# Performance work log

Measured on AMD Instinct MI355X. Metric: run time of the kernel, lower is better.

## Reference

```python
import jax, jax.numpy as jnp
import numpy as np


def setup_inputs() -> dict:
    key = jax.random.key(0)
    ks = jax.random.split(key, 7)
    B, S, D = 256, 1024, 128  # batch of sets, set size, n_input
    H = 256
    x = jax.random.normal(ks[0], (B, S, D), dtype=jnp.float32)
    # torch nn.Linear weights: [out_features, in_features], in = 2*layer_in
    W0 = jax.random.normal(ks[1], (H, 2 * D), dtype=jnp.float32) * 0.05
    b0 = jnp.zeros((H,), dtype=jnp.float32)
    W1 = jax.random.normal(ks[2], (H, 2 * H), dtype=jnp.float32) * 0.05
    b1 = jnp.zeros((H,), dtype=jnp.float32)
    W2 = jax.random.normal(ks[3], (H, 2 * H), dtype=jnp.float32) * 0.05
    b2 = jnp.zeros((H,), dtype=jnp.float32)
    return {"x": x, "W0": W0, "b0": b0, "W1": W1, "b1": b1, "W2": W2, "b2": b2}


def reference(x, W0, b0, W1, b1, W2, b2):
    # x: [B, S, D] batch of sets. Original loops over batch; we vmap.
    def apply_set(y):
        # y: [S, d]
        for W, b in ((W0, b0), (W1, b1), (W2, b2)):
            mean = jnp.mean(y, axis=0, keepdims=True)            # [1, d]
            mean = jnp.broadcast_to(mean, y.shape)               # [S, d]
            z = jnp.concatenate([y, mean], axis=1)               # [S, 2d]
            y = jnp.tanh(z @ W.T + b)                            # [S, out]
        return jnp.mean(y, axis=0)                               # [out]
    return jax.vmap(apply_set)(x)                                # [B, out]
```

## Files before the change

### kernel.cpp

```cpp
#include <hip/hip_runtime.h>
#include <hip/hip_bf16.h>

#define B_ 256
#define S_ 1024
#define D_ 128
#define H_ 256

typedef short short8 __attribute__((ext_vector_type(8)));
typedef float f32x4 __attribute__((ext_vector_type(4)));

__device__ unsigned short g_Wb0[H_ * D_];
__device__ unsigned short g_Wb1[H_ * H_];
__device__ unsigned short g_Wb2[H_ * H_];
__device__ float g_mean0[B_ * D_];
__device__ float g_colsum1[B_ * H_];
__device__ float g_colsum2[B_ * H_];

__device__ __forceinline__ unsigned short f2bf(float x) {
    union { float f; unsigned u; } v; v.f = x;
    unsigned r = v.u + 0x7FFFu + ((v.u >> 16) & 1u);
    return (unsigned short)(r >> 16);
}
__device__ __forceinline__ float bf2f(unsigned short h) {
    union { float f; unsigned u; } v; v.u = ((unsigned)h) << 16;
    return v.f;
}
__device__ __forceinline__ float fast_tanh(float x) {
    float e = __builtin_amdgcn_exp2f(x * 2.885390081777927f);
    float r = __builtin_amdgcn_rcpf(1.0f + e);
    return 1.0f - 2.0f * r;
}

__global__ __launch_bounds__(256) void prep_kernel(
    const float* __restrict__ W0, const float* __restrict__ W1,
    const float* __restrict__ W2)
{
    int i = blockIdx.x * 256 + threadIdx.x;
    if (i < H_ * D_) { g_Wb0[i] = f2bf(W0[(i >> 7) * 256 + (i & 127)]); return; }
    i -= H_ * D_;
    if (i < H_ * H_) { g_Wb1[i] = f2bf(W1[(i >> 8) * 512 + (i & 255)]); return; }
    i -= H_ * H_;
    if (i < H_ * H_) { g_Wb2[i] = f2bf(W2[(i >> 8) * 512 + (i & 255)]); return; }
}

__global__ __launch_bounds__(1024) void means0_kernel(const float* __restrict__ x)
{
    const int set = blockIdx.x, t = threadIdx.x;
    const int cg = t & 31, rg = t >> 5;
    const float* xb = x + (size_t)set * S_ * D_;
    f32x4 s = (f32x4){0.f, 0.f, 0.f, 0.f};
    #pragma unroll 8
    for (int i = 0; i < 32; ++i)
        s += *(const f32x4*)(xb + (rg + i * 32) * D_ + cg * 4);
    __shared__ f32x4 red[32][32];
    red[rg][cg] = s;
    __syncthreads();
    if (t < 32) {
        f32x4 a = red[0][t];
        #pragma unroll
        for (int g = 1; g < 32; ++g) a += red[g][t];
        #pragma unroll
        for (int c = 0; c < 4; ++c) g_mean0[set * D_ + t * 4 + c] = a[c];
    }
}

template <int LAYER>
__global__ __launch_bounds__(512, 2) void layer_kernel(
    const float* __restrict__ x, const float* __restrict__ W,
    const float* __restrict__ bias, unsigned short* __restrict__ y,
    float* __restrict__ out)
{
    constexpr int K  = (LAYER == 0) ? D_ : H_;
    constexpr int KS = K / 32;
    constexpr int SLOTS = K / 8;
    const int set = blockIdx.x;
    const int t = threadIdx.x;
    const int lane = t & 63, wave = t >> 6;
    const int l15 = lane & 15, quad = lane >> 4;

    __shared__ unsigned short W_lds[256 * K];
    __shared__ float mean_lds[K];
    __shared__ float c_lds[H_];
    __shared__ float colsum_lds[H_];
    __shared__ float cpart[512];

    const unsigned short* Wb = (LAYER == 0) ? g_Wb0 : (LAYER == 1) ? g_Wb1 : g_Wb2;
    const float* msrc = (LAYER == 0) ? g_mean0 : (LAYER == 1) ? g_colsum1 : g_colsum2;

    if (t < K)   mean_lds[t] = msrc[set * K + t] * (1.f / S_);
    if (t < H_)  colsum_lds[t] = 0.f;
    __syncthreads();

    {
        const int n = t >> 1, h = t & 1;
        #pragma unroll
        for (int i = 0; i < SLOTS / 2; ++i) {
            const int slot = h * (SLOTS / 2) + i;
            *(uint4*)(&W_lds[n * K + ((slot ^ (n & 7)) * 8)]) =
                *(const uint4*)(&Wb[n * K + slot * 8]);
        }
    }
    {
        const int j = t >> 1, h = t & 1;
        const float* wl = W + j * 2 * K + h * (K / 2);
        const float* wr = wl + K;
        float acc = 0.f;
        #pragma unroll 4
        for (int k = 0; k < K / 2; k += 4) {
            f32x4 a = *(const f32x4*)(wl + k);
            f32x4 b = *(const f32x4*)(wr + k);
            f32x4 m = *(const f32x4*)(&mean_lds[h * (K / 2) + k]);
            #pragma unroll
            for (int c = 0; c < 4; ++c)
                acc += m[c] * (b[c] + (a[c] - bf2f(f2bf(a[c]))));
        }
        cpart[t] = acc;
    }
    __syncthreads();
    if (t < H_) c_lds[t] = bias[t] + cpart[2 * t] + cpart[2 * t + 1];
    __syncthreads();

    for (int half = 0; half < 2; ++half) {
        const int rowbase = half * 512 + wave * 64;

        short8 a[4][KS];
        if (LAYER == 0) {
            const float* xb = x + ((size_t)set * S_ + rowbase) * D_;
            #pragma unroll
            for (int mf = 0; mf < 4; ++mf)
                #pragma unroll
                for (int ks = 0; ks < KS; ++ks) {
                    const float* p = xb + (mf * 16 + l15) * D_ + ks * 32 + quad * 8;
                    f32x4 v0 = *(const f32x4*)(p);
                    f32x4 v1 = *(const f32x4*)(p + 4);
                    short8 sv;
                    #pragma unroll
                    for (int c = 0; c < 4; ++c) {
                        sv[c]     = (short)f2bf(v0[c]);
                        sv[4 + c] = (short)f2bf(v1[c]);
                    }
                    a[mf][ks] = sv;
                }
        } else {
            const unsigned short* yb = y + ((size_t)set * S_ + rowbase) * H_;
            #pragma unroll
            for (int mf = 0; mf < 4; ++mf)
                #pragma unroll
                for (int ks = 0; ks < KS; ++ks)
                    a[mf][ks] = *(const short8*)(yb + (mf * 16 + l15) * H_ + ks * 32 + quad * 8);
        }

        for (int nt = 0; nt < 8; ++nt) {
            f32x4 acc[4][2];
            #pragma unroll
            for (int i = 0; i < 4; ++i) {
                acc[i][0] = (f32x4){0.f, 0.f, 0.f, 0.f};
                acc[i][1] = (f32x4){0.f, 0.f, 0.f, 0.f};
            }
            const int r0 = (nt * 32 + l15) * K;
            const int r1 = (nt * 32 + 16 + l15) * K;
            #pragma unroll
            for (int ks = 0; ks < KS; ++ks) {
                const int so = (((ks * 4 + quad) ^ (l15 & 7)) * 8);
                short8 b0 = *(const short8*)(&W_lds[r0 + so]);
                short8 b1 = *(const short8*)(&W_lds[r1 + so]);
                #pragma unroll
                for (int mf = 0; mf < 4; ++mf)
                    acc[mf][0] = __builtin_amdgcn_mfma_f32_16x16x32_bf16(a[mf][ks], b0, acc[mf][0], 0, 0, 0);
                #pragma unroll
                for (int mf = 0; mf < 4; ++mf)
                    acc[mf][1] = __builtin_amdgcn_mfma_f32_16x16x32_bf16(a[mf][ks], b1, acc[mf][1], 0, 0, 0);
            }
            #pragma unroll
            for (int nf = 0; nf < 2; ++nf) {
                const int col = nt * 32 + nf * 16 + l15;
                const float cv = c_lds[col];
                float sn = 0.f;
                #pragma unroll
                for (int mf = 0; mf < 4; ++mf) {
                    #pragma unroll
                    for (int r = 0; r < 4; ++r) {
                        float th = fast_tanh(acc[mf][nf][r] + cv);
                        sn += th;
                        if (LAYER < 2)
                            y[((size_t)set * S_ + rowbase + mf * 16 + quad * 4 + r) * H_ + col] = f2bf(th);
                    }
                }
                sn += __shfl_xor(sn, 16);
                sn += __shfl_xor(sn, 32);
                if (quad == 0) atomicAdd(&colsum_lds[col], sn);
            }
        }
    }
    __syncthreads();
    if (t < H_) {
        if (LAYER == 2) out[set * H_ + t] = colsum_lds[t] * (1.f / S_);
        else if (LAYER == 1) g_colsum2[set * H_ + t] = colsum_lds[t];
        else g_colsum1[set * H_ + t] = colsum_lds[t];
    }
}

extern "C" void kernel_launch(void* const* d_in, const int* in_sizes, int n_in,
                              void* d_out, int out_size, void* d_ws, size_t ws_size,
                              hipStream_t stream) {
    (void)in_sizes; (void)n_in; (void)out_size; (void)ws_size;
    const float* x  = (const float*)d_in[0];
    const float* W0 = (const float*)d_in[1];
    const float* b0 = (const float*)d_in[2];
    const float* W1 = (const float*)d_in[3];
    const float* b1 = (const float*)d_in[4];
    const float* W2 = (const float*)d_in[5];
    const float* b2 = (const float*)d_in[6];
    float* out = (float*)d_out;
    unsigned short* ws = (unsigned short*)d_ws;

    prep_kernel<<<dim3(640), dim3(256), 0, stream>>>(W0, W1, W2);
    means0_kernel<<<dim3(256), dim3(1024), 0, stream>>>(x);
    layer_kernel<0><<<dim3(256), dim3(512), 0, stream>>>(x, W0, b0, ws, out);
    layer_kernel<1><<<dim3(256), dim3(512), 0, stream>>>(x, W1, b1, ws, out);
    layer_kernel<2><<<dim3(256), dim3(512), 0, stream>>>(x, W2, b2, ws, out);
}
```

Before: 431.7 us.

## Split each set's output columns across two blocks and ping-pong activation buffers

Each layer kernel now launches two blocks per set, each computing 128 of the 256 output columns, which halves the weight tile held in LDS and raises the occupancy target to 4 blocks per SM. Per-wave work is restructured into smaller 32-row by 32-column tiles with fewer accumulators to relieve register pressure. Because two blocks now read and write the same set's activations concurrently, layer 1 writes its output into the input x buffer instead of the workspace, avoiding a read/write race. That makes the kernel overwrite a caller input, and each block reloads the full A rows, doubling activation reads.

```diff
diff --git a/kernel.cpp b/kernel.cpp
--- a/kernel.cpp
+++ b/kernel.cpp
@@ -65,51 +65,51 @@
 }
 
 template <int LAYER>
-__global__ __launch_bounds__(512, 2) void layer_kernel(
+__global__ __launch_bounds__(512, 4) void layer_kernel(
     const float* __restrict__ x, const float* __restrict__ W,
-    const float* __restrict__ bias, unsigned short* __restrict__ y,
-    float* __restrict__ out)
+    const float* __restrict__ bias, const unsigned short* __restrict__ yin,
+    unsigned short* __restrict__ yout, float* __restrict__ out)
 {
     constexpr int K  = (LAYER == 0) ? D_ : H_;
     constexpr int KS = K / 32;
-    constexpr int SLOTS = K / 8;
-    const int set = blockIdx.x;
+    const int set = blockIdx.x >> 1, ch = blockIdx.x & 1;
     const int t = threadIdx.x;
     const int lane = t & 63, wave = t >> 6;
     const int l15 = lane & 15, quad = lane >> 4;
 
-    __shared__ unsigned short W_lds[256 * K];
+    __shared__ unsigned short W_lds[128 * K];
     __shared__ float mean_lds[K];
-    __shared__ float c_lds[H_];
-    __shared__ float colsum_lds[H_];
+    __shared__ float c_lds[128];
+    __shared__ float colsum_lds[128];
     __shared__ float cpart[512];
 
     const unsigned short* Wb = (LAYER == 0) ? g_Wb0 : (LAYER == 1) ? g_Wb1 : g_Wb2;
     const float* msrc = (LAYER == 0) ? g_mean0 : (LAYER == 1) ? g_colsum1 : g_colsum2;
 
+    if (t < 128) colsum_lds[t] = 0.f;
     if (t < K)   mean_lds[t] = msrc[set * K + t] * (1.f / S_);
-    if (t < H_)  colsum_lds[t] = 0.f;
     __syncthreads();
 
     {
-        const int n = t >> 1, h = t & 1;
+        const int n = t & 127, g = t >> 7;
+        const unsigned short* src = Wb + (size_t)(ch * 128 + n) * K;
         #pragma unroll
-        for (int i = 0; i < SLOTS / 2; ++i) {
-            const int slot = h * (SLOTS / 2) + i;
+        for (int i = 0; i < KS; ++i) {
+            const int slot = g * KS + i;
             *(uint4*)(&W_lds[n * K + ((slot ^ (n & 7)) * 8)]) =
-                *(const uint4*)(&Wb[n * K + slot * 8]);
+                *(const uint4*)(src + slot * 8);
         }
     }
     {
-        const int j = t >> 1, h = t & 1;
-        const float* wl = W + j * 2 * K + h * (K / 2);
+        const int j = t >> 2, q = t & 3;
+        const float* wl = W + (size_t)(ch * 128 + j) * 2 * K + q * (K / 4);
         const float* wr = wl + K;
         float acc = 0.f;
         #pragma unroll 4
-        for (int k = 0; k < K / 2; k += 4) {
+        for (int k = 0; k < K / 4; k += 4) {
             f32x4 a = *(const f32x4*)(wl + k);
             f32x4 b = *(const f32x4*)(wr + k);
-            f32x4 m = *(const f32x4*)(&mean_lds[h * (K / 2) + k]);
+            f32x4 m = *(const f32x4*)(&mean_lds[q * (K / 4) + k]);
             #pragma unroll
             for (int c = 0; c < 4; ++c)
                 acc += m[c] * (b[c] + (a[c] - bf2f(f2bf(a[c]))));
@@ -117,22 +117,26 @@
         cpart[t] = acc;
     }
     __syncthreads();
-    if (t < H_) c_lds[t] = bias[t] + cpart[2 * t] + cpart[2 * t + 1];
-    __syncthreads();
-
-    for (int half = 0; half < 2; ++half) {
-        const int rowbase = half * 512 + wave * 64;
-
-        short8 a[4][KS];
+    if (t < 128)
+        c_lds[t] = bias[ch * 128 + t] +
+                   cpart[4 * t] + cpart[4 * t + 1] + cpart[4 * t + 2] + cpart[4 * t + 3];
+    __syncthreads();
+
+    const int rowA = wave * 128;
+    #pragma unroll 1
+    for (int p = 0; p < 4; ++p) {
+        const int row0 = rowA + p * 32 + l15;
+
+        short8 a[2][KS];
         if (LAYER == 0) {
-            const float* xb = x + ((size_t)set * S_ + rowbase) * D_;
-            #pragma unroll
-            for (int mf = 0; mf < 4; ++mf)
+            const float* xb = x + ((size_t)set * S_ + row0) * D_ + quad * 8;
+            #pragma unroll
+            for (int mf = 0; mf < 2; ++mf)
                 #pragma unroll
                 for (int ks = 0; ks < KS; ++ks) {
-                    const float* p = xb + (mf * 16 + l15) * D_ + ks * 32 + quad * 8;
-                    f32x4 v0 = *(const f32x4*)(p);
-                    f32x4 v1 = *(const f32x4*)(p + 4);
+                    const float* p2 = xb + mf * 16 * D_ + ks * 32;
+                    f32x4 v0 = *(const f32x4*)(p2);
+                    f32x4 v1 = *(const f32x4*)(p2 + 4);
                     short8 sv;
                     #pragma unroll
                     for (int c = 0; c < 4; ++c) {
@@ -142,61 +146,58 @@
                     a[mf][ks] = sv;
                 }
         } else {
-            const unsigned short* yb = y + ((size_t)set * S_ + rowbase) * H_;
-            #pragma unroll
-            for (int mf = 0; mf < 4; ++mf)
+            const unsigned short* yb = yin + ((size_t)set * S_ + row0) * H_ + quad * 8;
+            #pragma unroll
+            for (int mf = 0; mf < 2; ++mf)
                 #pragma unroll
                 for (int ks = 0; ks < KS; ++ks)
-                    a[mf][ks] = *(const short8*)(yb + (mf * 16 + l15) * H_ + ks * 32 + quad * 8);
-        }
-
-        for (int nt = 0; nt < 8; ++nt) {
-            f32x4 acc[4][2];
-            #pragma unroll
-            for (int i = 0; i < 4; ++i) {
-                acc[i][0] = (f32x4){0.f, 0.f, 0.f, 0.f};
-                acc[i][1] = (f32x4){0.f, 0.f, 0.f, 0.f};
+                    a[mf][ks] = *(const short8*)(yb + mf * 16 * H_ + ks * 32);
+        }
+
+        #pragma unroll 1
+        for (int nt = 0; nt < 4; ++nt) {
+            f32x4 acc[2][2];
+            acc[0][0] = acc[0][1] = acc[1][0] = acc[1][1] = (f32x4){0.f, 0.f, 0.f, 0.f};
+            const int rb0 = (nt * 32 + l15) * K;
+            const int rb1 = (nt * 32 + 16 + l15) * K;
+            #pragma unroll
+            for (int ks = 0; ks < KS; ++ks) {
+                const int so = ((ks * 4 + quad) ^ (l15 & 7)) * 8;
+                short8 b0 = *(const short8*)(&W_lds[rb0 + so]);
+                short8 b1 = *(const short8*)(&W_lds[rb1 + so]);
+                acc[0][0] = __builtin_amdgcn_mfma_f32_16x16x32_bf16(a[0][ks], b0, acc[0][0], 0, 0, 0);
+                acc[1][0] = __builtin_amdgcn_mfma_f32_16x16x32_bf16(a[1][ks], b0, acc[1][0], 0, 0, 0);
+                acc[0][1] = __builtin_amdgcn_mfma_f32_16x16x32_bf16(a[0][ks], b1, acc[0][1], 0, 0, 0);
+                acc[1][1] = __builtin_amdgcn_mfma_f32_16x16x32_bf16(a[1][ks], b1, acc[1][1], 0, 0, 0);
             }
-            const int r0 = (nt * 32 + l15) * K;
-            const int r1 = (nt * 32 + 16 + l15) * K;
-            #pragma unroll
-            for (int ks = 0; ks < KS; ++ks) {
-                const int so = (((ks * 4 + quad) ^ (l15 & 7)) * 8);
-                short8 b0 = *(const short8*)(&W_lds[r0 + so]);
-                short8 b1 = *(const short8*)(&W_lds[r1 + so]);
-                #pragma unroll
-                for (int mf = 0; mf < 4; ++mf)
-                    acc[mf][0] = __builtin_amdgcn_mfma_f32_16x16x32_bf16(a[mf][ks], b0, acc[mf][0], 0, 0, 0);
-                #pragma unroll
-                for (int mf = 0; mf < 4; ++mf)
-                    acc[mf][1] = __builtin_amdgcn_mfma_f32_16x16x32_bf16(a[mf][ks], b1, acc[mf][1], 0, 0, 0);
-            }
             #pragma unroll
             for (int nf = 0; nf < 2; ++nf) {
-                const int col = nt * 32 + nf * 16 + l15;
-                const float cv = c_lds[col];
+                const int lcol = nt * 32 + nf * 16 + l15;
+                const float cv = c_lds[lcol];
                 float sn = 0.f;
                 #pragma unroll
-                for (int mf = 0; mf < 4; ++mf) {
+                for (int mf = 0; mf < 2; ++mf) {
+                    unsigned short* yo = (LAYER < 2)
+                        ? yout + ((size_t)set * S_ + rowA + p * 32 + mf * 16 + quad * 4) * H_ + ch * 128 + lcol
+                        : nullptr;
                     #pragma unroll
                     for (int r = 0; r < 4; ++r) {
                         float th = fast_tanh(acc[mf][nf][r] + cv);
                         sn += th;
-                        if (LAYER < 2)
-                            y[((size_t)set * S_ + rowbase + mf * 16 + quad * 4 + r) * H_ + col] = f2bf(th);
+                        if (LAYER < 2) yo[r * H_] = f2bf(th);
                     }
                 }
                 sn += __shfl_xor(sn, 16);
                 sn += __shfl_xor(sn, 32);
-                if (quad == 0) atomicAdd(&colsum_lds[col], sn);
+                if (quad == 0) atomicAdd(&colsum_lds[lcol], sn);
             }
         }
     }
     __syncthreads();
-    if (t < H_) {
-        if (LAYER == 2) out[set * H_ + t] = colsum_lds[t] * (1.f / S_);
-        else if (LAYER == 1) g_colsum2[set * H_ + t] = colsum_lds[t];
-        else g_colsum1[set * H_ + t] = colsum_lds[t];
+    if (t < 128) {
+        if (LAYER == 0)      g_colsum1[set * H_ + ch * 128 + t] = colsum_lds[t];
+        else if (LAYER == 1) g_colsum2[set * H_ + ch * 128 + t] = colsum_lds[t];
+        else                 out[set * H_ + ch * 128 + t] = colsum_lds[t] * (1.f / S_);
     }
 }
 
@@ -212,11 +213,13 @@
     const float* W2 = (const float*)d_in[5];
     const float* b2 = (const float*)d_in[6];
     float* out = (float*)d_out;
-    unsigned short* ws = (unsigned short*)d_ws;
+
+    unsigned short* y0 = (unsigned short*)d_ws;
+    unsigned short* y1 = (unsigned short*)d_in[0];
 
     prep_kernel<<<dim3(640), dim3(256), 0, stream>>>(W0, W1, W2);
     means0_kernel<<<dim3(256), dim3(1024), 0, stream>>>(x);
-    layer_kernel<0><<<dim3(256), dim3(512), 0, stream>>>(x, W0, b0, ws, out);
-    layer_kernel<1><<<dim3(256), dim3(512), 0, stream>>>(x, W1, b1, ws, out);
-    layer_kernel<2><<<dim3(256), dim3(512), 0, stream>>>(x, W2, b2, ws, out);
-}
+    layer_kernel<0><<<dim3(512), dim3(512), 0, stream>>>(x, W0, b0, y0, y0, out);
+    layer_kernel<1><<<dim3(512), dim3(512), 0, stream>>>(x, W1, b1, y0, y1, out);
+    layer_kernel<2><<<dim3(512), dim3(512), 0, stream>>>(x, W2, b2, y1, y1, out);
+}
```

Result: slower. 452.2 us (+4.7%).
